# Kernel tuning notes

Measured on AMD Instinct MI355X. Metric: run time of the kernel, lower is better.

## Reference

```python
import jax, jax.numpy as jnp
import numpy as np

B, C, L = 8, 512, 512
MAX_LEN = 48
LAST_WIN = 64  # hard-coded final window in the torch module


def _fofe_all(x, alpha, max_len):
    """Windowed FOFE encoder.

    Torch semantics: out[:, :, i, t] = sum_{k=0}^{w_i-1} alpha^k * x[:, :, t-1-k]
    (zero outside [0, L-1]), for windows w_i = 0..max_len-1 plus w=64,
    produced there by per-window depthwise conv1d with left pad w.
    We compute it via the linear recurrence z[t] = alpha*z[t-1] + x[t]
    (associative scan) and the windowed identity
    out_w[t] = z[t-1] - alpha^w * z[t-1-w].
    """
    Bx, Cx, Lx = x.shape
    # per-channel decay broadcast over (B, C, L)
    a = jnp.broadcast_to(alpha[None, :, 0:1], x.shape)

    def comb(c1, c2):
        a1, b1 = c1
        a2, b2 = c2
        return (a1 * a2, a2 * b1 + b2)

    _, z = jax.lax.associative_scan(comb, (a, x), axis=-1)  # z[t] = sum_k alpha^k x[t-k]

    windows_i = jnp.concatenate([jnp.arange(max_len), jnp.array([LAST_WIN])])  # (nw,)
    windows_f = windows_i.astype(x.dtype)
    W = max(max_len - 1, LAST_WIN)  # largest left shift needed
    zp = jnp.pad(z, ((0, 0), (0, 0), (W + 1, 0)))  # zeros for negative time indices

    t = jnp.arange(Lx + 1)
    base = zp[:, :, W + t]  # z[t-1], shape (B, C, L+1)
    idx = t[None, :] + (W - windows_i[:, None])  # (nw, L+1), all >= 0
    shifted = zp[:, :, idx]  # z[t-1-w], shape (B, C, nw, L+1)
    ap = jnp.power(alpha, windows_f[None, :])  # (C, nw); alpha is (C,1)
    out = base[:, :, None, :] - ap[None, :, :, None] * shifted  # (B, C, nw, L+1)
    return out


def setup_inputs() -> dict:
    key = jax.random.key(0)
    kx, = jax.random.split(key, 1)
    x = jax.random.normal(kx, (B, C, L), dtype=jnp.float32)
    alpha = jnp.full((C, 1), 0.8, dtype=jnp.float32)  # learned per-channel decay, init 0.8
    return {"x": x, "alpha": alpha, "max_len": MAX_LEN}


def reference(x, alpha, max_len):
    return _fofe_all(x, alpha, max_len)
```

## Files before the change

kernel.cpp:

```cpp
#include <hip/hip_runtime.h>


#define CC 512
#define LL 512
#define NW 49
#define LO 513
#define NPAD 65
#define ZSZ 640

typedef float f32x4 __attribute__((ext_vector_type(4)));

__device__ __forceinline__ int swz(int i) { return i ^ ((i >> 5) & 3); }

__global__ __launch_bounds__(256, 4)
void fofe_kernel(const float* __restrict__ x,
                 const float* __restrict__ alpha,
                 float* __restrict__ out)
{
    __shared__ float zp[4][ZSZ];

    const int tid  = threadIdx.x;
    const int wid  = tid >> 6;
    const int lane = tid & 63;
    const int row  = blockIdx.x * 2 + (wid >> 1);
    const int half = wid & 1;
    const int c    = row & (CC - 1);

    const float al = alpha[c];
    const float* xr = x + (size_t)row * LL;

    const f32x4 xv0 = reinterpret_cast<const f32x4*>(xr)[lane * 2];
    const f32x4 xv1 = reinterpret_cast<const f32x4*>(xr)[lane * 2 + 1];
    const float xe[8] = {xv0.x, xv0.y, xv0.z, xv0.w,
                         xv1.x, xv1.y, xv1.z, xv1.w};

    float l[8];
    {
        float s = 0.f;
        #pragma unroll
        for (int m = 0; m < 8; ++m) { s = fmaf(al, s, xe[m]); l[m] = s; }
    }
    float pw[8];
    {
        float p = al;
        #pragma unroll
        for (int m = 0; m < 8; ++m) { pw[m] = p; p *= al; }
    }

    float A = pw[7];
    float S = l[7];
    #pragma unroll
    for (int off = 1; off < 64; off <<= 1) {
        const float Ap = __shfl_up(A, off);
        const float Sp = __shfl_up(S, off);
        if (lane >= off) { S = fmaf(A, Sp, S); A = A * Ap; }
    }
    float carry = __shfl_up(S, 1);
    if (lane == 0) carry = 0.f;

    float* z = zp[wid];
    z[swz(lane)] = 0.f;
    if (lane == 0) z[swz(64)] = 0.f;
    #pragma unroll
    for (int m = 0; m < 8; ++m)
        z[swz(NPAD + lane * 8 + m)] = fmaf(pw[m], carry, l[m]);

    const float al2 = al * al;
    const float a4  = al2 * al2;
    const float a8  = a4 * a4;
    const float a16 = a8 * a8;
    const float a64 = (a16 * a16) * (a16 * a16);
    float ap = half ? al : 1.0f;

    float* orow = out + (size_t)row * (NW * LO);

    for (int i = half; i < NW; i += 2) {
        const int   w   = (i < 48) ? i : 64;
        const float apw = (i < 48) ? ap : a64;
        float* op = orow + i * LO;
        const int q    = (row + i) & 3;
        const int peel = (4 - q) & 3;
        const int zb0  = NPAD - 1;

        if (lane < peel) {
            const int t = lane;
            op[t] = fmaf(-apw, z[swz(zb0 + t - w)], z[swz(zb0 + t)]);
        }

        const int nf4  = (LO - peel) >> 2;
        const int tail = (LO - peel) & 3;
        for (int f = lane; f < nf4; f += 64) {
            const int t0 = peel + 4 * f;
            f32x4 v;
            v.x = fmaf(-apw, z[swz(zb0 + t0     - w)], z[swz(zb0 + t0    )]);
            v.y = fmaf(-apw, z[swz(zb0 + t0 + 1 - w)], z[swz(zb0 + t0 + 1)]);
            v.z = fmaf(-apw, z[swz(zb0 + t0 + 2 - w)], z[swz(zb0 + t0 + 2)]);
            v.w = fmaf(-apw, z[swz(zb0 + t0 + 3 - w)], z[swz(zb0 + t0 + 3)]);
            *reinterpret_cast<f32x4*>(op + t0) = v;
        }

        if (lane < tail) {
            const int t = peel + 4 * nf4 + lane;
            op[t] = fmaf(-apw, z[swz(zb0 + t - w)], z[swz(zb0 + t)]);
        }
        ap *= al2;
    }
}

extern "C" void kernel_launch(void* const* d_in, const int* in_sizes, int n_in,
                              void* d_out, int out_size, void* d_ws, size_t ws_size,
                              hipStream_t stream)
{
    const float* x     = (const float*)d_in[0];
    const float* alpha = (const float*)d_in[1];
    float* out = (float*)d_out;

    const int rows = 8 * CC;
    const int grid = rows / 2;
    fofe_kernel<<<grid, 256, 0, stream>>>(x, alpha, out);
}
```

Measured before the change: 91.00 us.

## Switch to persistent 256-block grid processing 16 rows per block

Replaces the 2048-block launch (two rows per 256-thread block) with a persistent grid of 256 blocks of 512 threads. Each block first computes scans for 16 rows into shared memory, then the 8 waves cooperatively write each row's 49 output windows, with a barrier between rows. This is meant to cut block launch overhead and spread stores across all waves, at the cost of per-row barriers and a serialized scan phase before any output is written.

```diff
diff --git a/kernel.cpp b/kernel.cpp
--- a/kernel.cpp
+++ b/kernel.cpp
@@ -5,105 +5,115 @@
 #define LL 512
 #define NW 49
 #define LO 513
-#define NPAD 65
-#define ZSZ 640
+#define SLAB (NW * LO)
+#define GRID 256
+#define NTAU 16
+#define ZOFF 65
+#define ZROW 640
 
 typedef float f32x4 __attribute__((ext_vector_type(4)));
 
 __device__ __forceinline__ int swz(int i) { return i ^ ((i >> 5) & 3); }
 
-__global__ __launch_bounds__(256, 4)
+__global__ __launch_bounds__(512)
 void fofe_kernel(const float* __restrict__ x,
                  const float* __restrict__ alpha,
                  float* __restrict__ out)
 {
-    __shared__ float zp[4][ZSZ];
+    __shared__ float zs[NTAU][ZROW];
 
     const int tid  = threadIdx.x;
     const int wid  = tid >> 6;
     const int lane = tid & 63;
-    const int row  = blockIdx.x * 2 + (wid >> 1);
-    const int half = wid & 1;
-    const int c    = row & (CC - 1);
+    const int blk  = blockIdx.x;
 
-    const float al = alpha[c];
-    const float* xr = x + (size_t)row * LL;
+    for (int tau = wid; tau < NTAU; tau += 8) {
+        const int g = tau * GRID + blk;
+        const float al = alpha[g & (CC - 1)];
+        const float* xr = x + (size_t)g * LL;
 
-    const f32x4 xv0 = reinterpret_cast<const f32x4*>(xr)[lane * 2];
-    const f32x4 xv1 = reinterpret_cast<const f32x4*>(xr)[lane * 2 + 1];
-    const float xe[8] = {xv0.x, xv0.y, xv0.z, xv0.w,
-                         xv1.x, xv1.y, xv1.z, xv1.w};
+        const f32x4 xv0 = reinterpret_cast<const f32x4*>(xr)[lane * 2];
+        const f32x4 xv1 = reinterpret_cast<const f32x4*>(xr)[lane * 2 + 1];
+        const float xe[8] = {xv0.x, xv0.y, xv0.z, xv0.w,
+                             xv1.x, xv1.y, xv1.z, xv1.w};
+        float l[8];
+        {
+            float s = 0.f;
+            #pragma unroll
+            for (int m = 0; m < 8; ++m) { s = fmaf(al, s, xe[m]); l[m] = s; }
+        }
+        float pw[8];
+        {
+            float p = al;
+            #pragma unroll
+            for (int m = 0; m < 8; ++m) { pw[m] = p; p *= al; }
+        }
+        float A = pw[7], S = l[7];
+        #pragma unroll
+        for (int off = 1; off < 64; off <<= 1) {
+            const float Ap = __shfl_up(A, off);
+            const float Sp = __shfl_up(S, off);
+            if (lane >= off) { S = fmaf(A, Sp, S); A = A * Ap; }
+        }
+        float carry = __shfl_up(S, 1);
+        if (lane == 0) carry = 0.f;
 
-    float l[8];
-    {
-        float s = 0.f;
+        float* z = zs[tau];
+        z[swz(lane)] = 0.f;
+        if (lane == 0) z[swz(64)] = 0.f;
         #pragma unroll
-        for (int m = 0; m < 8; ++m) { s = fmaf(al, s, xe[m]); l[m] = s; }
+        for (int m = 0; m < 8; ++m)
+            z[swz(ZOFF + lane * 8 + m)] = fmaf(pw[m], carry, l[m]);
     }
-    float pw[8];
-    {
-        float p = al;
-        #pragma unroll
-        for (int m = 0; m < 8; ++m) { pw[m] = p; p *= al; }
-    }
+    __syncthreads();
 
-    float A = pw[7];
-    float S = l[7];
-    #pragma unroll
-    for (int off = 1; off < 64; off <<= 1) {
-        const float Ap = __shfl_up(A, off);
-        const float Sp = __shfl_up(S, off);
-        if (lane >= off) { S = fmaf(A, Sp, S); A = A * Ap; }
-    }
-    float carry = __shfl_up(S, 1);
-    if (lane == 0) carry = 0.f;
+    for (int tau = 0; tau < NTAU; ++tau) {
+        const int g = tau * GRID + blk;
+        const float al = alpha[g & (CC - 1)];
+        const float* z = zs[tau];
+        float* oslab = out + (size_t)g * SLAB;
 
-    float* z = zp[wid];
-    z[swz(lane)] = 0.f;
-    if (lane == 0) z[swz(64)] = 0.f;
-    #pragma unroll
-    for (int m = 0; m < 8; ++m)
-        z[swz(NPAD + lane * 8 + m)] = fmaf(pw[m], carry, l[m]);
+        const float a2  = al * al, a4 = a2 * a2, a8 = a4 * a4;
+        const float a16 = a8 * a8;
+        const float a64 = (a16 * a16) * (a16 * a16);
 
-    const float al2 = al * al;
-    const float a4  = al2 * al2;
-    const float a8  = a4 * a4;
-    const float a16 = a8 * a8;
-    const float a64 = (a16 * a16) * (a16 * a16);
-    float ap = half ? al : 1.0f;
-
-    float* orow = out + (size_t)row * (NW * LO);
-
-    for (int i = half; i < NW; i += 2) {
-        const int   w   = (i < 48) ? i : 64;
-        const float apw = (i < 48) ? ap : a64;
-        float* op = orow + i * LO;
-        const int q    = (row + i) & 3;
-        const int peel = (4 - q) & 3;
-        const int zb0  = NPAD - 1;
-
-        if (lane < peel) {
-            const int t = lane;
-            op[t] = fmaf(-apw, z[swz(zb0 + t - w)], z[swz(zb0 + t)]);
+        float p = 1.f;
+        {
+            float m = al;
+            #pragma unroll
+            for (int b = 0; b < 3; ++b) { if (wid & (1 << b)) p *= m; m *= m; }
         }
 
-        const int nf4  = (LO - peel) >> 2;
-        const int tail = (LO - peel) & 3;
-        for (int f = lane; f < nf4; f += 64) {
-            const int t0 = peel + 4 * f;
-            f32x4 v;
-            v.x = fmaf(-apw, z[swz(zb0 + t0     - w)], z[swz(zb0 + t0    )]);
-            v.y = fmaf(-apw, z[swz(zb0 + t0 + 1 - w)], z[swz(zb0 + t0 + 1)]);
-            v.z = fmaf(-apw, z[swz(zb0 + t0 + 2 - w)], z[swz(zb0 + t0 + 2)]);
-            v.w = fmaf(-apw, z[swz(zb0 + t0 + 3 - w)], z[swz(zb0 + t0 + 3)]);
-            *reinterpret_cast<f32x4*>(op + t0) = v;
+        for (int i = wid; i < NW; i += 8) {
+            const int   w   = (i < 48) ? i : 64;
+            const float apw = (i < 48) ? p : a64;
+            float* op = oslab + i * LO;
+            const int q    = (g + i) & 3;
+            const int peel = (4 - q) & 3;
+            const int k0b  = ZOFF - 1;
+
+            if (lane < peel)
+                op[lane] = fmaf(-apw, z[swz(k0b + lane - w)], z[swz(k0b + lane)]);
+
+            const int nf4  = (LO - peel) >> 2;
+            const int tail = (LO - peel) & 3;
+            for (int f = lane; f < nf4; f += 64) {
+                const int t0 = peel + 4 * f;
+                const int k0 = k0b + t0;
+                f32x4 v;
+                v.x = fmaf(-apw, z[swz(k0     - w)], z[swz(k0    )]);
+                v.y = fmaf(-apw, z[swz(k0 + 1 - w)], z[swz(k0 + 1)]);
+                v.z = fmaf(-apw, z[swz(k0 + 2 - w)], z[swz(k0 + 2)]);
+                v.w = fmaf(-apw, z[swz(k0 + 3 - w)], z[swz(k0 + 3)]);
+                *reinterpret_cast<f32x4*>(op + t0) = v;
+            }
+            if (lane < tail) {
+                const int t = peel + 4 * nf4 + lane;
+                op[t] = fmaf(-apw, z[swz(k0b + t - w)], z[swz(k0b + t)]);
+            }
+            p *= a8;
         }
-
-        if (lane < tail) {
-            const int t = peel + 4 * nf4 + lane;
-            op[t] = fmaf(-apw, z[swz(zb0 + t - w)], z[swz(zb0 + t)]);
-        }
-        ap *= al2;
+        __syncthreads();
     }
 }
 
@@ -115,7 +125,5 @@
     const float* alpha = (const float*)d_in[1];
     float* out = (float*)d_out;
 
-    const int rows = 8 * CC;
-    const int grid = rows / 2;
-    fofe_kernel<<<grid, 256, 0, stream>>>(x, alpha, out);
+    fofe_kernel<<<GRID, 512, 0, stream>>>(x, alpha, out);
 }
```

Result: faster. 85.90 us (-5.6%).
